# Performance work log

Hardware: AMD Instinct MI355X
Metric: run time of the kernel (lower is better)

## Reference

```python
import jax, jax.numpy as jnp
import numpy as np

L, H, D_IN, D_OUT, B, T = 64, 50, 60, 50, 32, 2048


def setup_inputs() -> dict:
    key = jax.random.key(0)
    ks = jax.random.split(key, 8)
    s = 1.0 / np.sqrt(H)  # torch LSTM init: U(-1/sqrt(H), 1/sqrt(H))
    u = lambda k, shp: jax.random.uniform(k, shp, jnp.float32, -s, s)
    return {
        "x": jax.random.normal(ks[0], (B, D_IN, T), jnp.float32),
        "hn": jnp.zeros((L, B, H), jnp.float32),
        "cn": jnp.zeros((L, B, H), jnp.float32),
        "W_ih0": u(ks[1], (4 * H, D_IN)),          # layer 0 input weights
        "W_ih": u(ks[2], (L - 1, 4 * H, H)),        # layers 1..63 input weights
        "W_hh": u(ks[3], (L, 4 * H, H)),
        "b_ih": u(ks[4], (L, 4 * H)),
        "b_hh": u(ks[5], (L, 4 * H)),
        "fc_w": u(ks[6], (D_OUT, H)),
        "fc_b": u(ks[7], (D_OUT,)),
    }


def _lstm_layer(xs, W_ih, W_hh, b, h0, c0):
    # xs: [T, B, D]; gate order i, f, g, o (PyTorch convention)
    def step(carry, xt):
        h, c = carry
        g = xt @ W_ih.T + h @ W_hh.T + b  # [B, 4H]
        i, f, gg, o = jnp.split(g, 4, axis=-1)
        c = jax.nn.sigmoid(f) * c + jax.nn.sigmoid(i) * jnp.tanh(gg)
        h = jax.nn.sigmoid(o) * jnp.tanh(c)
        return (h, c), h
    (hT, cT), ys = jax.lax.scan(step, (h0, c0), xs)
    return ys, hT, cT


def reference(x, hn, cn, W_ih0, W_ih, W_hh, b_ih, b_hh, fc_w, fc_b):
    xs = jnp.transpose(x, (2, 0, 1))  # [T, B, D_in]
    b = b_ih + b_hh  # [L, 4H]
    hs, cs = [], []
    ys, hT, cT = _lstm_layer(xs, W_ih0, W_hh[0], b[0], hn[0], cn[0])
    hs.append(hT); cs.append(cT)
    for l in range(1, L):  # inter-layer dropout omitted (eval mode)
        ys, hT, cT = _lstm_layer(ys, W_ih[l - 1], W_hh[l], b[l], hn[l], cn[l])
        hs.append(hT); cs.append(cT)
    out = jax.nn.sigmoid(ys @ fc_w.T + fc_b)      # [T, B, D_out]
    return jnp.transpose(out, (1, 2, 0)), jnp.stack(hs), jnp.stack(cs)
```

## Files before the change

kernel.cpp:

```cpp
#include <hip/hip_runtime.h>

#define NLAYER 64
#define HID    50
#define DIN    60
#define DOUT   50
#define BATCH  32
#define NT     2048
#define NG     200
#define DEPTH  16
#define BS     8

#define FLAGS_WORDS (NLAYER*4*NT)
#define CONS_WORDS  256
#define RING_ROW    52
#define RING_SLOT   (BATCH*RING_ROW)
#define RING_WORDS  ((size_t)63*DEPTH*RING_SLOT)
#define RING_OFF    ((size_t)(FLAGS_WORDS + CONS_WORDS)*4)
#define Y63_OFF     (RING_OFF + RING_WORDS*4)

#define HS_OFF ((size_t)BATCH*DOUT*NT)
#define CS_OFF (HS_OFF + (size_t)NLAYER*BATCH*HID)

typedef float f4 __attribute__((ext_vector_type(4)));

__device__ __forceinline__ unsigned llc_load_u32(const unsigned* p) {
  unsigned r;
  asm volatile("global_load_dword %0, %1, off sc0 sc1\n\ts_waitcnt vmcnt(0)"
               : "=v"(r) : "v"(p) : "memory");
  return r;
}
__device__ __forceinline__ void llc_store_u32(unsigned* p, unsigned v) {
  asm volatile("global_store_dword %0, %1, off sc0 sc1" :: "v"(p), "v"(v) : "memory");
}
__device__ __forceinline__ f4 llc_load_f4(const float* p) {
  f4 r;
  asm volatile("global_load_dwordx4 %0, %1, off sc0 sc1\n\ts_waitcnt vmcnt(0)"
               : "=v"(r) : "v"(p) : "memory");
  return r;
}
__device__ __forceinline__ void llc_store_f32(float* p, float v) {
  asm volatile("global_store_dword %0, %1, off sc0 sc1" :: "v"(p), "v"(v) : "memory");
}

__device__ __forceinline__ float sigf(float v)  { return 1.f / (1.f + __expf(-v)); }
__device__ __forceinline__ float tanhx(float v) { return 2.f / (1.f + __expf(-2.f*v)) - 1.f; }

__global__ __launch_bounds__(256, 1) void lstm_pipe(
    const float* __restrict__ x,   const float* __restrict__ hn,
    const float* __restrict__ cn,  const float* __restrict__ Wih0,
    const float* __restrict__ Wih, const float* __restrict__ Whh,
    const float* __restrict__ bih, const float* __restrict__ bhh,
    unsigned* flags, int* cons, float* ring, float* y63, float* out)
{
  __shared__ float h_lds[BS*52];
  __shared__ float x_lds[BS*64];
  __shared__ float g_lds[BS*NG];

  const int tid = threadIdx.x;
  const int bid = blockIdx.x;
  const int xcd = bid & 7, jj = bid >> 3;
  const int l = xcd*8 + (jj >> 2);
  const int q = jj & 3;

  float wih0[60], wih1[60], whh0[52], whh1[52];
  float bias0 = 0.f, bias1 = 0.f, c0 = 0.f, c1 = 0.f;
  const int p  = tid % 100, bh = tid / 100;
  const int r0 = 2*p, r1 = r0 + 1, b0 = bh*4;
  if (tid < 200) {
    const float *wr0, *wr1; int KX;
    if (l == 0) { wr0 = Wih0 + r0*DIN; wr1 = Wih0 + r1*DIN; KX = DIN; }
    else {
      wr0 = Wih + ((size_t)(l-1)*NG + r0)*HID;
      wr1 = Wih + ((size_t)(l-1)*NG + r1)*HID;
      KX = HID;
    }
#pragma unroll
    for (int k = 0; k < 60; ++k) {
      wih0[k] = (k < KX) ? wr0[k] : 0.f;
      wih1[k] = (k < KX) ? wr1[k] : 0.f;
    }
    const float* hr0 = Whh + ((size_t)l*NG + r0)*HID;
    const float* hr1 = Whh + ((size_t)l*NG + r1)*HID;
#pragma unroll
    for (int k = 0; k < 52; ++k) {
      whh0[k] = (k < HID) ? hr0[k] : 0.f;
      whh1[k] = (k < HID) ? hr1[k] : 0.f;
    }
    bias0 = bih[l*NG + r0] + bhh[l*NG + r0];
    bias1 = bih[l*NG + r1] + bhh[l*NG + r1];
    const int u1 = tid, u2 = tid + 200;
    c0 = cn[((size_t)l*BATCH + q*BS + u1/HID)*HID + u1%HID];
    c1 = cn[((size_t)l*BATCH + q*BS + u2/HID)*HID + u2%HID];
  }
  for (int idx = tid; idx < BS*52; idx += 256) {
    const int b = idx/52, j = idx%52;
    h_lds[idx] = (j < HID) ? hn[((size_t)l*BATCH + q*BS + b)*HID + j] : 0.f;
  }
  for (int idx = tid; idx < BS*64; idx += 256) x_lds[idx] = 0.f;
  __syncthreads();

  const unsigned* flag_in  = flags + ((l-1)*4 + q)*NT;
  unsigned*       flag_out = flags + (l*4 + q)*NT;
  int* cons_self = cons + (l*4 + q);
  int* cons_next = cons + ((l+1)*4 + q);

  for (int t = 0; t < NT; ++t) {
    const int slot = t & (DEPTH-1);
    if (tid == 0) {
      if (l > 0) {
        while (llc_load_u32(flag_in + t) == 0u) __builtin_amdgcn_s_sleep(1);
      }
      if (l < 63 && t >= DEPTH) {
        const int need = t - DEPTH + 1;
        while (__hip_atomic_load(cons_next, __ATOMIC_RELAXED, __HIP_MEMORY_SCOPE_AGENT) < need)
          __builtin_amdgcn_s_sleep(1);
      }
    }
    __syncthreads();

    if (l == 0) {
      for (int idx = tid; idx < BS*DIN; idx += 256) {
        const int b = idx/DIN, d = idx%DIN;
        x_lds[b*64 + d] = x[((size_t)(q*BS + b)*DIN + d)*NT + t];
      }
    } else {
      if (tid < 104) {
        const int b = tid/13, k4 = tid%13;
        f4 v = llc_load_f4(ring + (size_t)((l-1)*DEPTH + slot)*RING_SLOT
                                + (q*BS + b)*RING_ROW + k4*4);
        *(f4*)&x_lds[b*64 + k4*4] = v;
      }
    }
    __syncthreads();
    if (tid == 0 && l > 0)
      __hip_atomic_store(cons_self, t+1, __ATOMIC_RELAXED, __HIP_MEMORY_SCOPE_AGENT);

    if (tid < 200) {
      float a0[4], a1[4];
#pragma unroll
      for (int b = 0; b < 4; ++b) { a0[b] = bias0; a1[b] = bias1; }
#pragma unroll
      for (int k4 = 0; k4 < 15; ++k4) {
#pragma unroll
        for (int b = 0; b < 4; ++b) {
          f4 xv = *(const f4*)&x_lds[(b0+b)*64 + k4*4];
#pragma unroll
          for (int j = 0; j < 4; ++j) {
            a0[b] = fmaf(xv[j], wih0[4*k4+j], a0[b]);
            a1[b] = fmaf(xv[j], wih1[4*k4+j], a1[b]);
          }
        }
      }
#pragma unroll
      for (int k4 = 0; k4 < 13; ++k4) {
#pragma unroll
        for (int b = 0; b < 4; ++b) {
          f4 hv = *(const f4*)&h_lds[(b0+b)*52 + k4*4];
#pragma unroll
          for (int j = 0; j < 4; ++j) {
            a0[b] = fmaf(hv[j], whh0[4*k4+j], a0[b]);
            a1[b] = fmaf(hv[j], whh1[4*k4+j], a1[b]);
          }
        }
      }
#pragma unroll
      for (int b = 0; b < 4; ++b) {
        g_lds[(b0+b)*NG + r0] = a0[b];
        g_lds[(b0+b)*NG + r1] = a1[b];
      }
    }
    __syncthreads();

    if (tid < 200) {
#pragma unroll
      for (int half = 0; half < 2; ++half) {
        const int u = tid + half*200;
        const int b = u / HID, j = u % HID;
        const float cprev = half ? c1 : c0;
        const float gi = g_lds[b*NG + j];
        const float gf = g_lds[b*NG +  50 + j];
        const float gg = g_lds[b*NG + 100 + j];
        const float go = g_lds[b*NG + 150 + j];
        const float cc = sigf(gf)*cprev + sigf(gi)*tanhx(gg);
        const float hh = sigf(go)*tanhx(cc);
        if (half) c1 = cc; else c0 = cc;
        h_lds[b*52 + j] = hh;
        const int bg = q*BS + b;
        if (l < 63)
          llc_store_f32(ring + (size_t)(l*DEPTH + slot)*RING_SLOT + bg*RING_ROW + j, hh);
        else
          y63[((size_t)t*BATCH + bg)*HID + j] = hh;
        if (t == NT-1) {
          out[HS_OFF + (size_t)l*BATCH*HID + bg*HID + j] = hh;
          out[CS_OFF + (size_t)l*BATCH*HID + bg*HID + j] = cc;
        }
      }
    }
    __syncthreads();
    if (tid == 0 && l < 63) llc_store_u32(flag_out + t, 1u);
  }
}

__global__ __launch_bounds__(320, 1) void fc_kernel(
    const float* __restrict__ y63, const float* __restrict__ fcw,
    const float* __restrict__ fcb, float* __restrict__ out)
{
  __shared__ float y_lds[64*52];
  __shared__ float w_lds[50*52];
  __shared__ float b_lds[50];
  const int tid = threadIdx.x;
  const int b  = blockIdx.x >> 5;
  const int t0 = (blockIdx.x & 31) * 64;
  for (int idx = tid; idx < 64*52; idx += 320) {
    const int r = idx / 52, j = idx % 52;
    y_lds[idx] = (j < HID) ? y63[((size_t)(t0 + r)*BATCH + b)*HID + j] : 0.f;
  }
  for (int idx = tid; idx < 50*52; idx += 320) {
    const int r = idx / 52, j = idx % 52;
    w_lds[idx] = (j < HID) ? fcw[r*HID + j] : 0.f;
  }
  if (tid < 50) b_lds[tid] = fcb[tid];
  __syncthreads();
  const int toff = tid & 63, dg = tid >> 6;
  for (int d = dg; d < DOUT; d += 5) {
    float acc = b_lds[d];
#pragma unroll
    for (int j4 = 0; j4 < 13; ++j4) {
      f4 yv = *(const f4*)&y_lds[toff*52 + j4*4];
      f4 wv = *(const f4*)&w_lds[d*52 + j4*4];
#pragma unroll
      for (int j = 0; j < 4; ++j) acc = fmaf(yv[j], wv[j], acc);
    }
    out[((size_t)b*DOUT + d)*NT + t0 + toff] = 1.f / (1.f + __expf(-acc));
  }
}

extern "C" void kernel_launch(void* const* d_in, const int* in_sizes, int n_in,
                              void* d_out, int out_size, void* d_ws, size_t ws_size,
                              hipStream_t stream)
{
  const float* x    = (const float*)d_in[0];
  const float* hn   = (const float*)d_in[1];
  const float* cn   = (const float*)d_in[2];
  const float* Wih0 = (const float*)d_in[3];
  const float* Wih  = (const float*)d_in[4];
  const float* Whh  = (const float*)d_in[5];
  const float* bih  = (const float*)d_in[6];
  const float* bhh  = (const float*)d_in[7];
  const float* fcw  = (const float*)d_in[8];
  const float* fcb  = (const float*)d_in[9];
  float* out = (float*)d_out;

  unsigned* flags = (unsigned*)d_ws;
  int*      cons  = (int*)((char*)d_ws + (size_t)FLAGS_WORDS*4);
  float*    ring  = (float*)((char*)d_ws + RING_OFF);
  float*    y63   = (float*)((char*)d_ws + Y63_OFF);
  (void)cons; (void)in_sizes; (void)n_in; (void)out_size; (void)ws_size;

  hipMemsetAsync(d_ws, 0, RING_OFF, stream);

  hipLaunchKernelGGL(lstm_pipe, dim3(256), dim3(256), 0, stream,
                     x, hn, cn, Wih0, Wih, Whh, bih, bhh,
                     flags, (int*)((char*)d_ws + (size_t)FLAGS_WORDS*4), ring, y63, out);
  hipLaunchKernelGGL(fc_kernel, dim3(1024), dim3(320), 0, stream, y63, fcw, fcb, out);
}
```

Baseline: 12.18 ms.

## Restructure LSTM wavefront pipeline with counters, prefetch, and readlane broadcast

Replaces the per-timestep flag array with monotonic producer and consumer counters, and moves spin-waiting out of a single thread so every thread polls. The next timestep's input is prefetched two steps ahead, and each thread's h output is published to the ring one step late so the stores overlap compute. The matvec now has one thread per gate row, with x and h values broadcast from registers via readlane instead of per-thread LDS reads, which removes one barrier per step. Spin loops carry a fuel limit, which risks silent wrong results if a producer stalls longer than the limit.

```diff
diff --git a/kernel.cpp b/kernel.cpp
--- a/kernel.cpp
+++ b/kernel.cpp
@@ -9,186 +9,212 @@
 #define NG     200
 #define DEPTH  16
 #define BS     8
-
-#define FLAGS_WORDS (NLAYER*4*NT)
-#define CONS_WORDS  256
-#define RING_ROW    52
-#define RING_SLOT   (BATCH*RING_ROW)
-#define RING_WORDS  ((size_t)63*DEPTH*RING_SLOT)
-#define RING_OFF    ((size_t)(FLAGS_WORDS + CONS_WORDS)*4)
-#define Y63_OFF     (RING_OFF + RING_WORDS*4)
+#define FUEL   (1 << 16)
+
+#define RING_OFF   4096
+#define SLOT_F     512
+#define RING_BYTES ((size_t)256*DEPTH*SLOT_F*4)
+#define Y63_OFF    (RING_OFF + RING_BYTES)
 
 #define HS_OFF ((size_t)BATCH*DOUT*NT)
 #define CS_OFF (HS_OFF + (size_t)NLAYER*BATCH*HID)
 
 typedef float f4 __attribute__((ext_vector_type(4)));
-
-__device__ __forceinline__ unsigned llc_load_u32(const unsigned* p) {
-  unsigned r;
-  asm volatile("global_load_dword %0, %1, off sc0 sc1\n\ts_waitcnt vmcnt(0)"
-               : "=v"(r) : "v"(p) : "memory");
-  return r;
-}
-__device__ __forceinline__ void llc_store_u32(unsigned* p, unsigned v) {
-  asm volatile("global_store_dword %0, %1, off sc0 sc1" :: "v"(p), "v"(v) : "memory");
-}
-__device__ __forceinline__ f4 llc_load_f4(const float* p) {
-  f4 r;
-  asm volatile("global_load_dwordx4 %0, %1, off sc0 sc1\n\ts_waitcnt vmcnt(0)"
-               : "=v"(r) : "v"(p) : "memory");
-  return r;
-}
-__device__ __forceinline__ void llc_store_f32(float* p, float v) {
-  asm volatile("global_store_dword %0, %1, off sc0 sc1" :: "v"(p), "v"(v) : "memory");
-}
+typedef unsigned long long u64;
+
+#define AL(p)   __hip_atomic_load((p),  __ATOMIC_RELAXED, __HIP_MEMORY_SCOPE_AGENT)
+#define AS(p,v) __hip_atomic_store((p), (v), __ATOMIC_RELAXED, __HIP_MEMORY_SCOPE_AGENT)
 
 __device__ __forceinline__ float sigf(float v)  { return 1.f / (1.f + __expf(-v)); }
 __device__ __forceinline__ float tanhx(float v) { return 2.f / (1.f + __expf(-2.f*v)) - 1.f; }
+
+__device__ __forceinline__ float bcast(const f4& A, const f4& B, int c, int j) {
+  float s = (c < 64) ? A[j] : B[j];
+  return __uint_as_float(__builtin_amdgcn_readlane(__float_as_uint(s), c & 63));
+}
+
+template<int KX>
+__device__ __forceinline__ void dotk(const f4& A, const f4& B,
+                                     const float* __restrict__ w,
+                                     float* __restrict__ acc) {
+#pragma unroll
+  for (int k = 0; k < KX; ++k) {
+    const int c0 = k >> 2, j = k & 3;
+#pragma unroll
+    for (int b = 0; b < 8; ++b)
+      acc[b] = fmaf(bcast(A, B, b*16 + c0, j), w[k], acc[b]);
+  }
+}
 
 __global__ __launch_bounds__(256, 1) void lstm_pipe(
     const float* __restrict__ x,   const float* __restrict__ hn,
     const float* __restrict__ cn,  const float* __restrict__ Wih0,
     const float* __restrict__ Wih, const float* __restrict__ Whh,
     const float* __restrict__ bih, const float* __restrict__ bhh,
-    unsigned* flags, int* cons, float* ring, float* y63, float* out)
+    unsigned* prod, unsigned* cons, float* ring, float* y63, float* out)
 {
-  __shared__ float h_lds[BS*52];
-  __shared__ float x_lds[BS*64];
-  __shared__ float g_lds[BS*NG];
-
-  const int tid = threadIdx.x;
-  const int bid = blockIdx.x;
+  __shared__ f4 x4[128];
+  __shared__ f4 h4[128];
+  __shared__ float g_lds[8*NG];
+  float* x_lds = (float*)x4;
+  float* h_lds = (float*)h4;
+
+  const int tid  = threadIdx.x;
+  const int lane = tid & 63;
+  const int bid  = blockIdx.x;
   const int xcd = bid & 7, jj = bid >> 3;
   const int l = xcd*8 + (jj >> 2);
   const int q = jj & 3;
-
-  float wih0[60], wih1[60], whh0[52], whh1[52];
-  float bias0 = 0.f, bias1 = 0.f, c0 = 0.f, c1 = 0.f;
-  const int p  = tid % 100, bh = tid / 100;
-  const int r0 = 2*p, r1 = r0 + 1, b0 = bh*4;
-  if (tid < 200) {
-    const float *wr0, *wr1; int KX;
-    if (l == 0) { wr0 = Wih0 + r0*DIN; wr1 = Wih0 + r1*DIN; KX = DIN; }
-    else {
-      wr0 = Wih + ((size_t)(l-1)*NG + r0)*HID;
-      wr1 = Wih + ((size_t)(l-1)*NG + r1)*HID;
-      KX = HID;
-    }
-#pragma unroll
-    for (int k = 0; k < 60; ++k) {
-      wih0[k] = (k < KX) ? wr0[k] : 0.f;
-      wih1[k] = (k < KX) ? wr1[k] : 0.f;
-    }
-    const float* hr0 = Whh + ((size_t)l*NG + r0)*HID;
-    const float* hr1 = Whh + ((size_t)l*NG + r1)*HID;
-#pragma unroll
-    for (int k = 0; k < 52; ++k) {
-      whh0[k] = (k < HID) ? hr0[k] : 0.f;
-      whh1[k] = (k < HID) ? hr1[k] : 0.f;
-    }
-    bias0 = bih[l*NG + r0] + bhh[l*NG + r0];
-    bias1 = bih[l*NG + r1] + bhh[l*NG + r1];
+  const int r = tid;
+  const int KPAD = (l == 0) ? DIN : HID;
+
+  float wih[60], whh[50];
+  float bias_r = 0.f, c0 = 0.f, c1 = 0.f;
+  if (r < NG) {
+    if (l == 0) {
+#pragma unroll
+      for (int k = 0; k < 60; ++k) wih[k] = Wih0[r*DIN + k];
+    } else {
+      const float* wr = Wih + ((size_t)(l-1)*NG + r)*HID;
+#pragma unroll
+      for (int k = 0; k < 60; ++k) wih[k] = (k < HID) ? wr[k] : 0.f;
+    }
+    const float* hr = Whh + ((size_t)l*NG + r)*HID;
+#pragma unroll
+    for (int k = 0; k < 50; ++k) whh[k] = hr[k];
+    bias_r = bih[l*NG + r] + bhh[l*NG + r];
     const int u1 = tid, u2 = tid + 200;
     c0 = cn[((size_t)l*BATCH + q*BS + u1/HID)*HID + u1%HID];
     c1 = cn[((size_t)l*BATCH + q*BS + u2/HID)*HID + u2%HID];
-  }
-  for (int idx = tid; idx < BS*52; idx += 256) {
-    const int b = idx/52, j = idx%52;
+  } else {
+#pragma unroll
+    for (int k = 0; k < 60; ++k) wih[k] = 0.f;
+#pragma unroll
+    for (int k = 0; k < 50; ++k) whh[k] = 0.f;
+  }
+#pragma unroll
+  for (int k = 0; k < 60; ++k) asm volatile("" : "+v"(wih[k]));
+#pragma unroll
+  for (int k = 0; k < 50; ++k) asm volatile("" : "+v"(whh[k]));
+  asm volatile("" : "+v"(bias_r));
+
+  for (int idx = tid; idx < 512; idx += 256) {
+    const int b = idx >> 6, j = idx & 63;
     h_lds[idx] = (j < HID) ? hn[((size_t)l*BATCH + q*BS + b)*HID + j] : 0.f;
   }
-  for (int idx = tid; idx < BS*64; idx += 256) x_lds[idx] = 0.f;
+
+  const unsigned* prod_in   = prod + ((l-1)*4 + q);
+  unsigned*       prod_out  = prod + (l*4 + q);
+  unsigned*       cons_self = cons + (l*4 + q);
+  const unsigned* cons_next = cons + ((l+1)*4 + q);
+
+  float*       ring_out = ring + ((size_t)(l*4 + q))*DEPTH*SLOT_F;
+  const float* ring_in  = ring + ((size_t)((l-1)*4 + q))*DEPTH*SLOT_F;
+
+  const int e0 = 2*tid, e1 = e0 + 1;
+  const int d0_ = e0 & 63, d1_ = d0_ + 1, eb = e0 >> 6;
+
+  float fx0 = 0.f, fx1 = 0.f;
+  if (l == 0) {
+    x_lds[e0] = (d0_ < DIN) ? x[((size_t)(q*BS + eb)*DIN + d0_)*NT + 0] : 0.f;
+    x_lds[e1] = (d1_ < DIN) ? x[((size_t)(q*BS + eb)*DIN + d1_)*NT + 0] : 0.f;
+    fx0 = (d0_ < DIN) ? x[((size_t)(q*BS + eb)*DIN + d0_)*NT + 1] : 0.f;
+    fx1 = (d1_ < DIN) ? x[((size_t)(q*BS + eb)*DIN + d1_)*NT + 1] : 0.f;
+  } else {
+    const u64* rin64 = (const u64*)ring_in;
+    int fuel = FUEL;
+    while (AL(prod_in) < 1u && --fuel) __builtin_amdgcn_s_sleep(4);
+    u64 v0 = AL(rin64 + tid);
+    x_lds[e0] = (d0_ < HID) ? __uint_as_float((unsigned)v0) : 0.f;
+    x_lds[e1] = (d1_ < HID) ? __uint_as_float((unsigned)(v0 >> 32)) : 0.f;
+    fuel = FUEL;
+    while (AL(prod_in) < 2u && --fuel) __builtin_amdgcn_s_sleep(4);
+    u64 v1 = AL(rin64 + SLOT_F/2 + tid);
+    fx0 = __uint_as_float((unsigned)v1);
+    fx1 = __uint_as_float((unsigned)(v1 >> 32));
+    if (tid == 0) AS(cons_self, 2u);
+  }
   __syncthreads();
 
-  const unsigned* flag_in  = flags + ((l-1)*4 + q)*NT;
-  unsigned*       flag_out = flags + (l*4 + q)*NT;
-  int* cons_self = cons + (l*4 + q);
-  int* cons_next = cons + ((l+1)*4 + q);
+  unsigned c_c = 0;
+  float hh0 = 0.f, hh1 = 0.f;
 
   for (int t = 0; t < NT; ++t) {
-    const int slot = t & (DEPTH-1);
+    f4 vxA = x4[lane], vxB = x4[lane + 64];
+    f4 vhA = h4[lane], vhB = h4[lane + 64];
+
+    if (l < 63 && t >= 1) {
+      int fuel = FUEL;
+      while ((int)c_c < t - 16 && --fuel) {
+        c_c = AL(cons_next);
+        if ((int)c_c < t - 16) __builtin_amdgcn_s_sleep(4);
+      }
+      if (tid < NG) {
+        unsigned* sb = (unsigned*)(ring_out + ((t-1) & (DEPTH-1))*SLOT_F);
+        AS(sb + (tid/HID)*64     + tid%HID, __float_as_uint(hh0));
+        AS(sb + (tid/HID + 4)*64 + tid%HID, __float_as_uint(hh1));
+      }
+    }
+
+    unsigned p_c2 = 0, c_c2 = c_c;
+    if (l > 0 && t + 2 < NT) p_c2 = AL(prod_in);
+    if (l < 63)              c_c2 = AL(cons_next);
+
+    float acc[8];
+#pragma unroll
+    for (int b = 0; b < 8; ++b) acc[b] = bias_r;
+    if (l == 0) dotk<60>(vxA, vxB, wih, acc);
+    else        dotk<50>(vxA, vxB, wih, acc);
+    dotk<50>(vhA, vhB, whh, acc);
+    if (r < NG) {
+#pragma unroll
+      for (int b = 0; b < 8; ++b) g_lds[b*NG + r] = acc[b];
+    }
+    __syncthreads();
+
+    if (t + 1 < NT) {
+      x_lds[e0] = (d0_ < KPAD) ? fx0 : 0.f;
+      x_lds[e1] = (d1_ < KPAD) ? fx1 : 0.f;
+    }
+
     if (tid == 0) {
-      if (l > 0) {
-        while (llc_load_u32(flag_in + t) == 0u) __builtin_amdgcn_s_sleep(1);
+      if (l < 63 && t >= 1) AS(prod_out, (unsigned)t);
+      if (l > 0)            AS(cons_self, (unsigned)(t + 2));
+    }
+
+    if (t + 2 < NT) {
+      if (l == 0) {
+        fx0 = (d0_ < DIN) ? x[((size_t)(q*BS + eb)*DIN + d0_)*NT + (t+2)] : 0.f;
+        fx1 = (d1_ < DIN) ? x[((size_t)(q*BS + eb)*DIN + d1_)*NT + (t+2)] : 0.f;
+      } else {
+        int fuel = FUEL;
+        while (p_c2 < (unsigned)(t + 3) && --fuel) {
+          p_c2 = AL(prod_in);
+          if (p_c2 < (unsigned)(t + 3)) __builtin_amdgcn_s_sleep(4);
+        }
+        const u64* lb = (const u64*)(ring_in + ((t+2) & (DEPTH-1))*SLOT_F);
+        u64 v = AL(lb + tid);
+        fx0 = __uint_as_float((unsigned)v);
+        fx1 = __uint_as_float((unsigned)(v >> 32));
       }
-      if (l < 63 && t >= DEPTH) {
-        const int need = t - DEPTH + 1;
-        while (__hip_atomic_load(cons_next, __ATOMIC_RELAXED, __HIP_MEMORY_SCOPE_AGENT) < need)
-          __builtin_amdgcn_s_sleep(1);
-      }
-    }
-    __syncthreads();
-
-    if (l == 0) {
-      for (int idx = tid; idx < BS*DIN; idx += 256) {
-        const int b = idx/DIN, d = idx%DIN;
-        x_lds[b*64 + d] = x[((size_t)(q*BS + b)*DIN + d)*NT + t];
-      }
-    } else {
-      if (tid < 104) {
-        const int b = tid/13, k4 = tid%13;
-        f4 v = llc_load_f4(ring + (size_t)((l-1)*DEPTH + slot)*RING_SLOT
-                                + (q*BS + b)*RING_ROW + k4*4);
-        *(f4*)&x_lds[b*64 + k4*4] = v;
-      }
-    }
-    __syncthreads();
-    if (tid == 0 && l > 0)
-      __hip_atomic_store(cons_self, t+1, __ATOMIC_RELAXED, __HIP_MEMORY_SCOPE_AGENT);
-
-    if (tid < 200) {
-      float a0[4], a1[4];
-#pragma unroll
-      for (int b = 0; b < 4; ++b) { a0[b] = bias0; a1[b] = bias1; }
-#pragma unroll
-      for (int k4 = 0; k4 < 15; ++k4) {
-#pragma unroll
-        for (int b = 0; b < 4; ++b) {
-          f4 xv = *(const f4*)&x_lds[(b0+b)*64 + k4*4];
-#pragma unroll
-          for (int j = 0; j < 4; ++j) {
-            a0[b] = fmaf(xv[j], wih0[4*k4+j], a0[b]);
-            a1[b] = fmaf(xv[j], wih1[4*k4+j], a1[b]);
-          }
-        }
-      }
-#pragma unroll
-      for (int k4 = 0; k4 < 13; ++k4) {
-#pragma unroll
-        for (int b = 0; b < 4; ++b) {
-          f4 hv = *(const f4*)&h_lds[(b0+b)*52 + k4*4];
-#pragma unroll
-          for (int j = 0; j < 4; ++j) {
-            a0[b] = fmaf(hv[j], whh0[4*k4+j], a0[b]);
-            a1[b] = fmaf(hv[j], whh1[4*k4+j], a1[b]);
-          }
-        }
-      }
-#pragma unroll
-      for (int b = 0; b < 4; ++b) {
-        g_lds[(b0+b)*NG + r0] = a0[b];
-        g_lds[(b0+b)*NG + r1] = a1[b];
-      }
-    }
-    __syncthreads();
-
-    if (tid < 200) {
+    }
+
+    if (tid < NG) {
 #pragma unroll
       for (int half = 0; half < 2; ++half) {
         const int u = tid + half*200;
         const int b = u / HID, j = u % HID;
         const float cprev = half ? c1 : c0;
-        const float gi = g_lds[b*NG + j];
-        const float gf = g_lds[b*NG +  50 + j];
-        const float gg = g_lds[b*NG + 100 + j];
-        const float go = g_lds[b*NG + 150 + j];
+        const float gi = g_lds[b*NG +            j];
+        const float gf = g_lds[b*NG +  50 +      j];
+        const float gg = g_lds[b*NG + 100 +      j];
+        const float go = g_lds[b*NG + 150 +      j];
         const float cc = sigf(gf)*cprev + sigf(gi)*tanhx(gg);
         const float hh = sigf(go)*tanhx(cc);
-        if (half) c1 = cc; else c0 = cc;
-        h_lds[b*52 + j] = hh;
+        if (half) { c1 = cc; hh1 = hh; } else { c0 = cc; hh0 = hh; }
+        h_lds[b*64 + j] = hh;
         const int bg = q*BS + b;
-        if (l < 63)
-          llc_store_f32(ring + (size_t)(l*DEPTH + slot)*RING_SLOT + bg*RING_ROW + j, hh);
-        else
+        if (l == 63)
           y63[((size_t)t*BATCH + bg)*HID + j] = hh;
         if (t == NT-1) {
           out[HS_OFF + (size_t)l*BATCH*HID + bg*HID + j] = hh;
@@ -196,8 +222,23 @@
         }
       }
     }
+    c_c = c_c2;
     __syncthreads();
-    if (tid == 0 && l < 63) llc_store_u32(flag_out + t, 1u);
+  }
+
+  if (l < 63) {
+    int fuel = FUEL;
+    while ((int)c_c < NT - 16 && --fuel) {
+      c_c = AL(cons_next);
+      if ((int)c_c < NT - 16) __builtin_amdgcn_s_sleep(4);
+    }
+    if (tid < NG) {
+      unsigned* sb = (unsigned*)(ring_out + ((NT-1) & (DEPTH-1))*SLOT_F);
+      AS(sb + (tid/HID)*64     + tid%HID, __float_as_uint(hh0));
+      AS(sb + (tid/HID + 4)*64 + tid%HID, __float_as_uint(hh1));
+    }
+    __syncthreads();
+    if (tid == 0) AS(prod_out, (unsigned)NT);
   }
 }
 
@@ -212,12 +253,12 @@
   const int b  = blockIdx.x >> 5;
   const int t0 = (blockIdx.x & 31) * 64;
   for (int idx = tid; idx < 64*52; idx += 320) {
-    const int r = idx / 52, j = idx % 52;
-    y_lds[idx] = (j < HID) ? y63[((size_t)(t0 + r)*BATCH + b)*HID + j] : 0.f;
+    const int rr = idx / 52, j = idx % 52;
+    y_lds[idx] = (j < HID) ? y63[((size_t)(t0 + rr)*BATCH + b)*HID + j] : 0.f;
   }
   for (int idx = tid; idx < 50*52; idx += 320) {
-    const int r = idx / 52, j = idx % 52;
-    w_lds[idx] = (j < HID) ? fcw[r*HID + j] : 0.f;
+    const int rr = idx / 52, j = idx % 52;
+    w_lds[idx] = (j < HID) ? fcw[rr*HID + j] : 0.f;
   }
   if (tid < 50) b_lds[tid] = fcb[tid];
   __syncthreads();
@@ -251,16 +292,16 @@
   const float* fcb  = (const float*)d_in[9];
   float* out = (float*)d_out;
 
-  unsigned* flags = (unsigned*)d_ws;
-  int*      cons  = (int*)((char*)d_ws + (size_t)FLAGS_WORDS*4);
-  float*    ring  = (float*)((char*)d_ws + RING_OFF);
-  float*    y63   = (float*)((char*)d_ws + Y63_OFF);
-  (void)cons; (void)in_sizes; (void)n_in; (void)out_size; (void)ws_size;
-
-  hipMemsetAsync(d_ws, 0, RING_OFF, stream);
+  unsigned* prod = (unsigned*)d_ws;
+  unsigned* cons = (unsigned*)((char*)d_ws + 1024);
+  float*    ring = (float*)((char*)d_ws + RING_OFF);
+  float*    y63  = (float*)((char*)d_ws + Y63_OFF);
+  (void)in_sizes; (void)n_in; (void)out_size; (void)ws_size;
+
+  hipMemsetAsync(d_ws, 0, 4096, stream);
 
   hipLaunchKernelGGL(lstm_pipe, dim3(256), dim3(256), 0, stream,
                      x, hn, cn, Wih0, Wih, Whh, bih, bhh,
-                     flags, (int*)((char*)d_ws + (size_t)FLAGS_WORDS*4), ring, y63, out);
+                     prod, cons, ring, y63, out);
   hipLaunchKernelGGL(fc_kernel, dim3(1024), dim3(320), 0, stream, y63, fcw, fcb, out);
 }
```

After: 17.20 ms. +41.2%, slower.
